# Kernel optimization log

Hardware: AMD Instinct MI355X
Metric: run time of the kernel (lower is better)

The kernel has to match this reference:

```python
import jax, jax.numpy as jnp
import numpy as np

N = 20000        # nodes
E = 320000       # edges (avg degree 16)
NHID = 256       # hidden dim (decoder input features)
NFEAT = 256      # reconstructed attribute dim
K_SELECTED = 4096  # number of nodes with label == 1 (static for jit)


def setup_inputs() -> dict:
    key = jax.random.key(0)
    ks = jax.random.split(key, 12)
    feature_attribute = jax.random.normal(ks[0], (N, NHID), dtype=jnp.float32)
    edge_row = jax.random.randint(ks[1], (E,), 0, N, dtype=jnp.int32)
    edge_col = jax.random.randint(ks[2], (E,), 0, N, dtype=jnp.int32)
    # positive, roughly degree-normalized adjacency weights
    edge_w = jax.random.uniform(ks[3], (E,), dtype=jnp.float32) / 16.0
    # first K_SELECTED nodes are labeled 1, rest 0 (static count for jit)
    labels = jnp.concatenate([jnp.ones((K_SELECTED,), jnp.int32),
                              jnp.zeros((N - K_SELECTED,), jnp.int32)])
    stdv1 = 1.0 / np.sqrt(NHID)
    stdv2 = 1.0 / np.sqrt(NFEAT)
    W1_ad = jax.random.uniform(ks[4], (NHID, NHID), minval=-stdv1, maxval=stdv1, dtype=jnp.float32)
    b1_ad = jax.random.uniform(ks[5], (NHID,), minval=-stdv1, maxval=stdv1, dtype=jnp.float32)
    W2_ad = jax.random.uniform(ks[6], (NHID, NFEAT), minval=-stdv2, maxval=stdv2, dtype=jnp.float32)
    b2_ad = jax.random.uniform(ks[7], (NFEAT,), minval=-stdv2, maxval=stdv2, dtype=jnp.float32)
    W_sd = jax.random.uniform(ks[8], (NHID, NHID), minval=-stdv1, maxval=stdv1, dtype=jnp.float32)
    b_sd = jax.random.uniform(ks[9], (NHID,), minval=-stdv1, maxval=stdv1, dtype=jnp.float32)
    return dict(feature_attribute=feature_attribute, edge_row=edge_row, edge_col=edge_col,
                edge_w=edge_w, labels=labels, W1_ad=W1_ad, b1_ad=b1_ad,
                W2_ad=W2_ad, b2_ad=b2_ad, W_sd=W_sd, b_sd=b_sd)


def reference(feature_attribute, edge_row, edge_col, edge_w, labels,
              W1_ad, b1_ad, W2_ad, b2_ad, W_sd, b_sd):
    def gcn(x, W, b):
        support = x @ W                                   # [N, d_out] dense mm
        msg = support[edge_col] * edge_w[:, None]         # gather + scale [E, d_out]
        out = jax.ops.segment_sum(msg, edge_row, num_segments=N)  # spmm aggregation
        return out + b

    # static-size index of labeled nodes (labels==1 count is K_SELECTED)
    idx = jnp.nonzero(labels == 1, size=K_SELECTED)[0]

    # Attribute decoder: relu(gc1) -> (dropout, eval: identity) -> gc2 -> select
    h = jax.nn.relu(gcn(feature_attribute, W1_ad, b1_ad))
    pred_attribute_mat = gcn(h, W2_ad, b2_ad)[idx]        # [K, NFEAT]

    # Structure decoder: gc1 -> select -> x @ x.T
    s = gcn(feature_attribute, W_sd, b_sd)[idx]           # [K, NHID]
    pred_adj_mat = s @ s.T                                # [K, K]

    return pred_attribute_mat, pred_adj_mat
```

## Files before the change

### kernel.cpp

```cpp
#include <hip/hip_runtime.h>
#include <hip/hip_bf16.h>

#define NN   20000
#define NE   320000
#define KSEL 4096

typedef short bf16x8 __attribute__((ext_vector_type(8)));
typedef float f32x4  __attribute__((ext_vector_type(4)));

static __device__ __forceinline__ float bf2f(unsigned short u){
  return __uint_as_float(((unsigned int)u) << 16);
}
static __device__ __forceinline__ unsigned short f2bf(float f){
  unsigned int x = __float_as_uint(f);
  x += 0x7fffu + ((x >> 16) & 1u);
  return (unsigned short)(x >> 16);
}
static __device__ __forceinline__ void gld_lds16(const unsigned short* g, unsigned short* l){
  __builtin_amdgcn_global_load_lds(
      (const __attribute__((address_space(1))) unsigned int*)g,
      (__attribute__((address_space(3))) unsigned int*)l, 16, 0, 0);
}

__global__ __launch_bounds__(256) void k_prep(const float* __restrict__ X,
    const float* __restrict__ W1, const float* __restrict__ Wsd, const float* __restrict__ W2,
    const int* __restrict__ labels,
    unsigned short* __restrict__ Xb, unsigned short* __restrict__ Wt,
    int* __restrict__ counts, int* __restrict__ partA){
  int b = blockIdx.x, tid = threadIdx.x;
  if (b < 2500){
    int i = (b * 256 + tid) * 8;
    float4 v0 = *(const float4*)(X + i);
    float4 v1 = *(const float4*)(X + i + 4);
    bf16x8 o;
    o[0] = (short)f2bf(v0.x); o[1] = (short)f2bf(v0.y);
    o[2] = (short)f2bf(v0.z); o[3] = (short)f2bf(v0.w);
    o[4] = (short)f2bf(v1.x); o[5] = (short)f2bf(v1.y);
    o[6] = (short)f2bf(v1.z); o[7] = (short)f2bf(v1.w);
    *(bf16x8*)(Xb + i) = o;
  } else if (b < 2548){
    __shared__ unsigned short lt[64 * 65];
    int b2 = b - 2500;
    int w = b2 >> 4, t = b2 & 15;
    int tR = (t >> 2) * 64, tC = (t & 3) * 64;
    const float* W = (w == 0) ? W1 : (w == 1 ? Wsd : W2);
    #pragma unroll
    for (int it = 0; it < 16; ++it){
      int lin = it * 256 + tid;
      int r = lin >> 6, c = lin & 63;
      lt[c * 65 + r] = f2bf(W[(size_t)(tR + r) * 256 + tC + c]);
    }
    __syncthreads();
    #pragma unroll
    for (int it = 0; it < 16; ++it){
      int lin = it * 256 + tid;
      int o = lin >> 6, k = lin & 63;
      Wt[(size_t)w * 65536 + (size_t)(tC + o) * 256 + tR + k] = lt[o * 65 + k];
    }
  } else {
    __shared__ int ws[4];
    int z = b - 2548, lane = tid & 63, wv = tid >> 6;
    if (tid < 250) *(int4*)&counts[z * 1000 + tid * 4] = make_int4(0, 0, 0, 0);
    int base = z * 1024 + tid * 4;
    int s = 0;
    #pragma unroll
    for (int j = 0; j < 4; ++j){
      int n0 = base + j;
      if (n0 < NN) s += (labels[n0] == 1) ? 1 : 0;
    }
    #pragma unroll
    for (int off = 32; off; off >>= 1) s += __shfl_down(s, off, 64);
    if (lane == 0) ws[wv] = s;
    __syncthreads();
    if (tid == 0) partA[z] = ws[0] + ws[1] + ws[2] + ws[3];
  }
}

__global__ __launch_bounds__(256) void k_hist_idx(const int* __restrict__ row,
    const int* __restrict__ labels, const int* __restrict__ partA,
    int* __restrict__ counts, int* __restrict__ idx){
  int tid = threadIdx.x;
  if (blockIdx.x < 1250){
    int e = blockIdx.x * 256 + tid;
    atomicAdd(&counts[row[e]], 1);
    return;
  }
  __shared__ int ws[4];
  __shared__ int boff_s;
  int bx = blockIdx.x - 1250;
  int lane = tid & 63, wv = tid >> 6;
  if (tid < 64){
    int v = (lane < 20) ? partA[lane] : 0;
    int acc = v;
    #pragma unroll
    for (int off = 1; off < 32; off <<= 1){
      int t = __shfl_up(acc, off, 64);
      if (lane >= off) acc += t;
    }
    if (lane == bx) boff_s = acc - v;
  }
  int base = bx * 1024 + tid * 4;
  int c[4]; int s = 0;
  #pragma unroll
  for (int j = 0; j < 4; ++j){
    int n0 = base + j;
    c[j] = (n0 < NN && labels[n0] == 1) ? 1 : 0;
    s += c[j];
  }
  int incl = s;
  #pragma unroll
  for (int off = 1; off < 64; off <<= 1){
    int t = __shfl_up(incl, off, 64);
    if (lane >= off) incl += t;
  }
  if (lane == 63) ws[wv] = incl;
  __syncthreads();
  int woff = boff_s;
  for (int w = 0; w < wv; ++w) woff += ws[w];
  int off = woff + incl - s;
  #pragma unroll
  for (int j = 0; j < 4; ++j){
    if (c[j]){ if (off < KSEL) idx[off] = base + j; ++off; }
  }
}

__global__ __launch_bounds__(256) void k_row_emit(const int* __restrict__ counts,
    int* __restrict__ start, int* __restrict__ cursor){
  __shared__ int ws[4];
  __shared__ int red[4];
  int tid = threadIdx.x, lane = tid & 63, wv = tid >> 6;
  int base = blockIdx.x * 1024;
  int ps = 0;
  for (int i = tid * 4; i < base; i += 1024){
    int4 v = *(const int4*)&counts[i];
    ps += v.x + v.y + v.z + v.w;
  }
  #pragma unroll
  for (int off = 32; off; off >>= 1) ps += __shfl_down(ps, off, 64);
  if (lane == 0) red[wv] = ps;
  __syncthreads();
  int bpref = red[0] + red[1] + red[2] + red[3];
  int nb = base + tid * 4;
  int c[4]; int s = 0;
  #pragma unroll
  for (int j = 0; j < 4; ++j){
    int n0 = nb + j;
    c[j] = (n0 < NN) ? counts[n0] : 0;
    s += c[j];
  }
  int incl = s;
  #pragma unroll
  for (int off = 1; off < 64; off <<= 1){
    int t = __shfl_up(incl, off, 64);
    if (lane >= off) incl += t;
  }
  if (lane == 63) ws[wv] = incl;
  __syncthreads();
  int woff = bpref;
  for (int w = 0; w < wv; ++w) woff += ws[w];
  int run = woff + incl - s;
  #pragma unroll
  for (int j = 0; j < 4; ++j){
    int n0 = nb + j;
    if (n0 < NN){ start[n0] = run; cursor[n0] = run; run += c[j]; }
  }
  if (blockIdx.x == 0 && tid == 0) start[NN] = NE;
}

__global__ void k_scatter(const int* __restrict__ row, const int* __restrict__ col,
                          const float* __restrict__ ew, int* __restrict__ cursor,
                          int2* __restrict__ rec){
  int e = blockIdx.x * 256 + threadIdx.x;
  if (e < NE){
    int r = row[e];
    int p = atomicAdd(&cursor[r], 1);
    rec[p] = make_int2(col[e], __float_as_int(ew[e]));
  }
}

__global__ __launch_bounds__(256) void k_spmm_full(const unsigned short* __restrict__ Xb,
    const int* __restrict__ start, const int2* __restrict__ rec,
    unsigned short* __restrict__ aggX){
  int wave = threadIdx.x >> 6, lane = threadIdx.x & 63;
  int half = lane >> 5, hl = lane & 31;
  int n = blockIdx.x * 4 + wave;
  int s = start[n], e = start[n + 1];
  int d = hl * 8;
  float acc[8] = {};
  for (int base = s; base < e; base += 64){
    int p = base + lane;
    int pc = p < e ? p : e - 1;
    int2 r = rec[pc];
    float wv = (p < e) ? __int_as_float(r.y) : 0.0f;
    int m = e - base; if (m > 64) m = 64;
    for (int j = 0; j < m; j += 8){
      int j0 = j + half, j1 = j + 2 + half, j2 = j + 4 + half, j3 = j + 6 + half;
      int   c0 = __shfl(r.x, j0), c1 = __shfl(r.x, j1);
      int   c2 = __shfl(r.x, j2), c3 = __shfl(r.x, j3);
      float w0 = __shfl(wv, j0),  w1 = __shfl(wv, j1);
      float w2 = __shfl(wv, j2),  w3 = __shfl(wv, j3);
      bf16x8 v0 = *(const bf16x8*)&Xb[(size_t)c0 * 256 + d];
      bf16x8 v1 = *(const bf16x8*)&Xb[(size_t)c1 * 256 + d];
      bf16x8 v2 = *(const bf16x8*)&Xb[(size_t)c2 * 256 + d];
      bf16x8 v3 = *(const bf16x8*)&Xb[(size_t)c3 * 256 + d];
      #pragma unroll
      for (int q = 0; q < 8; ++q){
        acc[q] += w0 * bf2f((unsigned short)v0[q]) + w1 * bf2f((unsigned short)v1[q])
                + w2 * bf2f((unsigned short)v2[q]) + w3 * bf2f((unsigned short)v3[q]);
      }
    }
  }
  #pragma unroll
  for (int q = 0; q < 8; ++q){
    float o = __shfl(acc[q], hl + 32);
    acc[q] += o;
  }
  if (half == 0){
    bf16x8 ob;
    #pragma unroll
    for (int q = 0; q < 8; ++q) ob[q] = (short)f2bf(acc[q]);
    *(bf16x8*)&aggX[(size_t)n * 256 + d] = ob;
  }
}

__global__ __launch_bounds__(256) void k_gemm_h(const unsigned short* __restrict__ A,
                                                const unsigned short* __restrict__ Wt,
                                                const float* __restrict__ bias,
                                                unsigned short* __restrict__ out, int M){
  __shared__ unsigned short At[128 * 64];
  __shared__ unsigned short Bt[64 * 64];
  int tid = threadIdx.x, wave = tid >> 6, lane = tid & 63;
  int lm = lane & 15, lq = lane >> 4;
  int mBase = blockIdx.x * 128;
  int oBase = blockIdx.y * 64;
  f32x4 acc[2][4] = {};
  for (int kc = 0; kc < 256; kc += 64){
    if (kc) __syncthreads();
    #pragma unroll
    for (int it = 0; it < 4; ++it){
      int s = (wave * 4 + it) * 64 + lane;
      int row = s >> 3, c = (s & 7) ^ (row & 7);
      int gr = mBase + row; if (gr >= M) gr = M - 1;
      gld_lds16(&A[(size_t)gr * 256 + kc + c * 8], &At[s * 8]);
    }
    #pragma unroll
    for (int it = 0; it < 2; ++it){
      int s = (wave * 2 + it) * 64 + lane;
      int row = s >> 3, c = (s & 7) ^ (row & 7);
      gld_lds16(&Wt[(size_t)(oBase + row) * 256 + kc + c * 8], &Bt[s * 8]);
    }
    __syncthreads();
    #pragma unroll
    for (int ks = 0; ks < 64; ks += 32){
      int cb = ks >> 3;
      int RA = wave * 32 + lm;
      int ca = ((cb + lq) ^ (RA & 7)) << 3;
      bf16x8 a0 = *(const bf16x8*)&At[RA * 64 + ca];
      bf16x8 a1 = *(const bf16x8*)&At[(RA + 16) * 64 + ca];
      #pragma unroll
      for (int os = 0; os < 4; ++os){
        int RB = os * 16 + lm;
        bf16x8 b = *(const bf16x8*)&Bt[RB * 64 + (((cb + lq) ^ (RB & 7)) << 3)];
        acc[0][os] = __builtin_amdgcn_mfma_f32_16x16x32_bf16(a0, b, acc[0][os], 0, 0, 0);
        acc[1][os] = __builtin_amdgcn_mfma_f32_16x16x32_bf16(a1, b, acc[1][os], 0, 0, 0);
      }
    }
  }
  #pragma unroll
  for (int ms = 0; ms < 2; ++ms){
    int rb = mBase + wave * 32 + ms * 16 + lq * 4;
    #pragma unroll
    for (int os = 0; os < 4; ++os){
      int col = oBase + os * 16 + lm;
      float bv = bias[col];
      #pragma unroll
      for (int r = 0; r < 4; ++r){
        int row = rb + r;
        if (row < M) out[(size_t)row * 256 + col] = f2bf(fmaxf(acc[ms][os][r] + bv, 0.f));
      }
    }
  }
}

__global__ __launch_bounds__(256) void k_spmm_selH(const unsigned short* __restrict__ h,
    const int* __restrict__ idx, const int* __restrict__ start, const int2* __restrict__ rec,
    unsigned short* __restrict__ aggH){
  int wave = threadIdx.x >> 6, lane = threadIdx.x & 63;
  int half = lane >> 5, hl = lane & 31;
  int i = blockIdx.x * 4 + wave;
  int n = idx[i];
  int s = start[n], e = start[n + 1];
  int d = hl * 8;
  float acc[8] = {};
  for (int base = s; base < e; base += 64){
    int p = base + lane;
    int pc = p < e ? p : e - 1;
    int2 r = rec[pc];
    float wv = (p < e) ? __int_as_float(r.y) : 0.0f;
    int m = e - base; if (m > 64) m = 64;
    for (int j = 0; j < m; j += 8){
      int j0 = j + half, j1 = j + 2 + half, j2 = j + 4 + half, j3 = j + 6 + half;
      int   c0 = __shfl(r.x, j0), c1 = __shfl(r.x, j1);
      int   c2 = __shfl(r.x, j2), c3 = __shfl(r.x, j3);
      float w0 = __shfl(wv, j0),  w1 = __shfl(wv, j1);
      float w2 = __shfl(wv, j2),  w3 = __shfl(wv, j3);
      bf16x8 v0 = *(const bf16x8*)&h[(size_t)c0 * 256 + d];
      bf16x8 v1 = *(const bf16x8*)&h[(size_t)c1 * 256 + d];
      bf16x8 v2 = *(const bf16x8*)&h[(size_t)c2 * 256 + d];
      bf16x8 v3 = *(const bf16x8*)&h[(size_t)c3 * 256 + d];
      #pragma unroll
      for (int q = 0; q < 8; ++q){
        acc[q] += w0 * bf2f((unsigned short)v0[q]) + w1 * bf2f((unsigned short)v1[q])
                + w2 * bf2f((unsigned short)v2[q]) + w3 * bf2f((unsigned short)v3[q]);
      }
    }
  }
  #pragma unroll
  for (int q = 0; q < 8; ++q){
    float o = __shfl(acc[q], hl + 32);
    acc[q] += o;
  }
  if (half == 0){
    bf16x8 ob;
    #pragma unroll
    for (int q = 0; q < 8; ++q) ob[q] = (short)f2bf(acc[q]);
    *(bf16x8*)&aggH[(size_t)i * 256 + d] = ob;
  }
}

__global__ __launch_bounds__(256) void k_gemm_os(const unsigned short* __restrict__ aggH,
    const unsigned short* __restrict__ aggX, const int* __restrict__ idx,
    const unsigned short* __restrict__ Wt,
    const float* __restrict__ b2, const float* __restrict__ bsd,
    float* __restrict__ out0, unsigned short* __restrict__ sel){
  __shared__ unsigned short lds[64 * 264];
  int tid = threadIdx.x;
  int wave = tid >> 6, lane = tid & 63;
  int lm = lane & 15, lq = lane >> 4;
  int z = blockIdx.z;
  int mBase = blockIdx.x * 128;
  int oBase = blockIdx.y * 64;
  const unsigned short* Wt2 = Wt + (z ? 256 * 256 : 512 * 256);
  const float* bias = z ? bsd : b2;
  #pragma unroll
  for (int it = 0; it < 8; ++it){
    int c = it * 256 + tid;
    int o = c >> 5, kk = (c & 31) << 3;
    *(bf16x8*)&lds[o * 264 + kk] = *(const bf16x8*)&Wt2[(oBase + o) * 256 + kk];
  }
  __syncthreads();
  int r0 = mBase + wave * 32 + lm;
  const unsigned short* A0;
  const unsigned short* A1;
  if (z){
    A0 = aggX + (size_t)idx[r0] * 256;
    A1 = aggX + (size_t)idx[r0 + 16] * 256;
  } else {
    A0 = aggH + (size_t)r0 * 256;
    A1 = aggH + (size_t)(r0 + 16) * 256;
  }
  f32x4 acc[2][4] = {};
  #pragma unroll
  for (int ks = 0; ks < 256; ks += 32){
    int ka = ks + lq * 8;
    bf16x8 a0 = *(const bf16x8*)&A0[ka];
    bf16x8 a1 = *(const bf16x8*)&A1[ka];
    #pragma unroll
    for (int os = 0; os < 4; ++os){
      bf16x8 b = *(const bf16x8*)&lds[(os * 16 + lm) * 264 + ka];
      acc[0][os] = __builtin_amdgcn_mfma_f32_16x16x32_bf16(a0, b, acc[0][os], 0, 0, 0);
      acc[1][os] = __builtin_amdgcn_mfma_f32_16x16x32_bf16(a1, b, acc[1][os], 0, 0, 0);
    }
  }
  #pragma unroll
  for (int ms = 0; ms < 2; ++ms){
    int rb = mBase + wave * 32 + ms * 16 + lq * 4;
    #pragma unroll
    for (int os = 0; os < 4; ++os){
      int col = oBase + os * 16 + lm;
      float bv = bias[col];
      #pragma unroll
      for (int r = 0; r < 4; ++r){
        float v = acc[ms][os][r] + bv;
        if (z) sel[(size_t)(rb + r) * 256 + col] = f2bf(v);
        else   out0[(size_t)(rb + r) * 256 + col] = v;
      }
    }
  }
}

__global__ __launch_bounds__(256) void k_gemm_st(const unsigned short* __restrict__ S,
                                                 float* __restrict__ out1){
  __shared__ unsigned short At[128 * 64];
  __shared__ unsigned short Bt[128 * 64];
  int tid = threadIdx.x, wave = tid >> 6, lane = tid & 63;
  int lm = lane & 15, lq = lane >> 4;
  int mBase = blockIdx.x * 128;
  int oBase = blockIdx.y * 128;
  f32x4 acc[2][8] = {};
  for (int kc = 0; kc < 256; kc += 64){
    if (kc) __syncthreads();
    #pragma unroll
    for (int it = 0; it < 4; ++it){
      int s = (wave * 4 + it) * 64 + lane;
      int row = s >> 3, c = (s & 7) ^ (row & 7);
      gld_lds16(&S[(size_t)(mBase + row) * 256 + kc + c * 8], &At[s * 8]);
      gld_lds16(&S[(size_t)(oBase + row) * 256 + kc + c * 8], &Bt[s * 8]);
    }
    __syncthreads();
    #pragma unroll
    for (int ks = 0; ks < 64; ks += 32){
      int cb = ks >> 3;
      int RA = wave * 32 + lm;
      int ca = ((cb + lq) ^ (RA & 7)) << 3;
      bf16x8 a0 = *(const bf16x8*)&At[RA * 64 + ca];
      bf16x8 a1 = *(const bf16x8*)&At[(RA + 16) * 64 + ca];
      #pragma unroll
      for (int os = 0; os < 8; ++os){
        int RB = os * 16 + lm;
        bf16x8 b = *(const bf16x8*)&Bt[RB * 64 + (((cb + lq) ^ (RB & 7)) << 3)];
        acc[0][os] = __builtin_amdgcn_mfma_f32_16x16x32_bf16(a0, b, acc[0][os], 0, 0, 0);
        acc[1][os] = __builtin_amdgcn_mfma_f32_16x16x32_bf16(a1, b, acc[1][os], 0, 0, 0);
      }
    }
  }
  #pragma unroll
  for (int ms = 0; ms < 2; ++ms){
    int rb = mBase + wave * 32 + ms * 16 + lq * 4;
    #pragma unroll
    for (int os = 0; os < 8; ++os){
      int col = oBase + os * 16 + lm;
      #pragma unroll
      for (int r = 0; r < 4; ++r)
        out1[(size_t)(rb + r) * 4096 + col] = acc[ms][os][r];
    }
  }
}

extern "C" void kernel_launch(void* const* d_in, const int* in_sizes, int n_in,
                              void* d_out, int out_size, void* d_ws, size_t ws_size,
                              hipStream_t stream){
  const float* X    = (const float*)d_in[0];
  const int*   erow = (const int*)d_in[1];
  const int*   ecol = (const int*)d_in[2];
  const float* ew   = (const float*)d_in[3];
  const int*   labels = (const int*)d_in[4];
  const float* W1   = (const float*)d_in[5];
  const float* b1   = (const float*)d_in[6];
  const float* W2   = (const float*)d_in[7];
  const float* b2   = (const float*)d_in[8];
  const float* Wsd  = (const float*)d_in[9];
  const float* bsd  = (const float*)d_in[10];
  float* out0 = (float*)d_out;
  float* out1 = out0 + (size_t)KSEL * 256;

  char* ws = (char*)d_ws;
  unsigned short* Xb   = (unsigned short*)(ws);
  unsigned short* Wt   = (unsigned short*)(ws + 10240000);
  unsigned short* aggX = (unsigned short*)(ws + 10633216);
  unsigned short* h    = (unsigned short*)(ws + 20873216);
  unsigned short* aggH = (unsigned short*)(ws + 31113216);
  unsigned short* sel  = (unsigned short*)(ws + 33210368);
  int* idx    = (int*)(ws + 35307520);
  int* counts = (int*)(ws + 35323904);
  int* startp = (int*)(ws + 35403904);
  int* cursor = (int*)(ws + 35483908);
  int2* rec   = (int2*)(ws + 35563912);
  int* partA  = (int*)(ws + 38123912);

  k_prep<<<2568, 256, 0, stream>>>(X, W1, Wsd, W2, labels, Xb, Wt, counts, partA);
  k_hist_idx<<<1270, 256, 0, stream>>>(erow, labels, partA, counts, idx);
  k_row_emit<<<20, 256, 0, stream>>>(counts, startp, cursor);
  k_scatter<<<NE / 256, 256, 0, stream>>>(erow, ecol, ew, cursor, rec);
  k_spmm_full<<<5000, 256, 0, stream>>>(Xb, startp, rec, aggX);
  k_gemm_h<<<dim3(157, 4), 256, 0, stream>>>(aggX, Wt, b1, h, NN);
  k_spmm_selH<<<1024, 256, 0, stream>>>(h, idx, startp, rec, aggH);
  k_gemm_os<<<dim3(32, 4, 2), 256, 0, stream>>>(aggH, aggX, idx, Wt, b2, bsd, out0, sel);
  k_gemm_st<<<dim3(32, 32), 256, 0, stream>>>(sel, out1);
}
```

Measured before the change: 203.8 us.

## Merge kernels into fewer launches and exploit Gram-matrix symmetry

The setup kernels are regrouped so that the X-to-bf16 conversion, the edge histogram and the index compaction run in one launch, with the weight transpose split into a small separate kernel. The selected-row Wsd GEMM is fused into the selected SpMM launch, and the W2 output GEMM into the S·Sᵀ launch. The K×K Gram matrix now computes only lower-triangular 128×128 tiles and writes each off-diagonal tile a second time in transposed form through LDS. These changes remove launch gaps and about half of the Gram-matrix MFMA work. The fused output GEMMs now read B directly from global memory instead of staging it in LDS, which may cost some bandwidth.

```diff
diff --git a/kernel.cpp b/kernel.cpp
--- a/kernel.cpp
+++ b/kernel.cpp
@@ -22,11 +22,52 @@
       (__attribute__((address_space(3))) unsigned int*)l, 16, 0, 0);
 }
 
-__global__ __launch_bounds__(256) void k_prep(const float* __restrict__ X,
-    const float* __restrict__ W1, const float* __restrict__ Wsd, const float* __restrict__ W2,
+__global__ __launch_bounds__(256) void k_prep0(const float* __restrict__ W1,
+    const float* __restrict__ Wsd, const float* __restrict__ W2,
     const int* __restrict__ labels,
-    unsigned short* __restrict__ Xb, unsigned short* __restrict__ Wt,
-    int* __restrict__ counts, int* __restrict__ partA){
+    unsigned short* __restrict__ Wt, int* __restrict__ counts, int* __restrict__ partA){
+  int b = blockIdx.x, tid = threadIdx.x;
+  if (b < 48){
+    __shared__ unsigned short lt[64 * 65];
+    int w = b >> 4, t = b & 15;
+    int tR = (t >> 2) * 64, tC = (t & 3) * 64;
+    const float* W = (w == 0) ? W1 : (w == 1 ? Wsd : W2);
+    #pragma unroll
+    for (int it = 0; it < 16; ++it){
+      int lin = it * 256 + tid;
+      int r = lin >> 6, c = lin & 63;
+      lt[c * 65 + r] = f2bf(W[(size_t)(tR + r) * 256 + tC + c]);
+    }
+    __syncthreads();
+    #pragma unroll
+    for (int it = 0; it < 16; ++it){
+      int lin = it * 256 + tid;
+      int o = lin >> 6, k = lin & 63;
+      Wt[(size_t)w * 65536 + (size_t)(tC + o) * 256 + tR + k] = lt[o * 65 + k];
+    }
+  } else {
+    __shared__ int ws[4];
+    int z = b - 48, lane = tid & 63, wv = tid >> 6;
+    if (tid < 250) *(int4*)&counts[z * 1000 + tid * 4] = make_int4(0, 0, 0, 0);
+    int base = z * 1024 + tid * 4;
+    int s = 0;
+    #pragma unroll
+    for (int j = 0; j < 4; ++j){
+      int n0 = base + j;
+      if (n0 < NN) s += (labels[n0] == 1) ? 1 : 0;
+    }
+    #pragma unroll
+    for (int off = 32; off; off >>= 1) s += __shfl_down(s, off, 64);
+    if (lane == 0) ws[wv] = s;
+    __syncthreads();
+    if (tid == 0) partA[z] = ws[0] + ws[1] + ws[2] + ws[3];
+  }
+}
+
+__global__ __launch_bounds__(256) void k_main1(const float* __restrict__ X,
+    const int* __restrict__ row, const int* __restrict__ labels,
+    const int* __restrict__ partA,
+    unsigned short* __restrict__ Xb, int* __restrict__ counts, int* __restrict__ idx){
   int b = blockIdx.x, tid = threadIdx.x;
   if (b < 2500){
     int i = (b * 256 + tid) * 8;
@@ -38,89 +79,47 @@
     o[4] = (short)f2bf(v1.x); o[5] = (short)f2bf(v1.y);
     o[6] = (short)f2bf(v1.z); o[7] = (short)f2bf(v1.w);
     *(bf16x8*)(Xb + i) = o;
-  } else if (b < 2548){
-    __shared__ unsigned short lt[64 * 65];
-    int b2 = b - 2500;
-    int w = b2 >> 4, t = b2 & 15;
-    int tR = (t >> 2) * 64, tC = (t & 3) * 64;
-    const float* W = (w == 0) ? W1 : (w == 1 ? Wsd : W2);
-    #pragma unroll
-    for (int it = 0; it < 16; ++it){
-      int lin = it * 256 + tid;
-      int r = lin >> 6, c = lin & 63;
-      lt[c * 65 + r] = f2bf(W[(size_t)(tR + r) * 256 + tC + c]);
-    }
-    __syncthreads();
-    #pragma unroll
-    for (int it = 0; it < 16; ++it){
-      int lin = it * 256 + tid;
-      int o = lin >> 6, k = lin & 63;
-      Wt[(size_t)w * 65536 + (size_t)(tC + o) * 256 + tR + k] = lt[o * 65 + k];
-    }
+  } else if (b < 3750){
+    int e = (b - 2500) * 256 + tid;
+    atomicAdd(&counts[row[e]], 1);
   } else {
     __shared__ int ws[4];
-    int z = b - 2548, lane = tid & 63, wv = tid >> 6;
-    if (tid < 250) *(int4*)&counts[z * 1000 + tid * 4] = make_int4(0, 0, 0, 0);
-    int base = z * 1024 + tid * 4;
-    int s = 0;
+    __shared__ int boff_s;
+    int bx = b - 3750;
+    int lane = tid & 63, wv = tid >> 6;
+    if (tid < 64){
+      int v = (lane < 20) ? partA[lane] : 0;
+      int acc = v;
+      #pragma unroll
+      for (int off = 1; off < 32; off <<= 1){
+        int t = __shfl_up(acc, off, 64);
+        if (lane >= off) acc += t;
+      }
+      if (lane == bx) boff_s = acc - v;
+    }
+    int base = bx * 1024 + tid * 4;
+    int c[4]; int s = 0;
     #pragma unroll
     for (int j = 0; j < 4; ++j){
       int n0 = base + j;
-      if (n0 < NN) s += (labels[n0] == 1) ? 1 : 0;
-    }
-    #pragma unroll
-    for (int off = 32; off; off >>= 1) s += __shfl_down(s, off, 64);
-    if (lane == 0) ws[wv] = s;
-    __syncthreads();
-    if (tid == 0) partA[z] = ws[0] + ws[1] + ws[2] + ws[3];
-  }
-}
-
-__global__ __launch_bounds__(256) void k_hist_idx(const int* __restrict__ row,
-    const int* __restrict__ labels, const int* __restrict__ partA,
-    int* __restrict__ counts, int* __restrict__ idx){
-  int tid = threadIdx.x;
-  if (blockIdx.x < 1250){
-    int e = blockIdx.x * 256 + tid;
-    atomicAdd(&counts[row[e]], 1);
-    return;
-  }
-  __shared__ int ws[4];
-  __shared__ int boff_s;
-  int bx = blockIdx.x - 1250;
-  int lane = tid & 63, wv = tid >> 6;
-  if (tid < 64){
-    int v = (lane < 20) ? partA[lane] : 0;
-    int acc = v;
-    #pragma unroll
-    for (int off = 1; off < 32; off <<= 1){
-      int t = __shfl_up(acc, off, 64);
-      if (lane >= off) acc += t;
-    }
-    if (lane == bx) boff_s = acc - v;
-  }
-  int base = bx * 1024 + tid * 4;
-  int c[4]; int s = 0;
-  #pragma unroll
-  for (int j = 0; j < 4; ++j){
-    int n0 = base + j;
-    c[j] = (n0 < NN && labels[n0] == 1) ? 1 : 0;
-    s += c[j];
-  }
-  int incl = s;
-  #pragma unroll
-  for (int off = 1; off < 64; off <<= 1){
-    int t = __shfl_up(incl, off, 64);
-    if (lane >= off) incl += t;
-  }
-  if (lane == 63) ws[wv] = incl;
-  __syncthreads();
-  int woff = boff_s;
-  for (int w = 0; w < wv; ++w) woff += ws[w];
-  int off = woff + incl - s;
-  #pragma unroll
-  for (int j = 0; j < 4; ++j){
-    if (c[j]){ if (off < KSEL) idx[off] = base + j; ++off; }
+      c[j] = (n0 < NN && labels[n0] == 1) ? 1 : 0;
+      s += c[j];
+    }
+    int incl = s;
+    #pragma unroll
+    for (int off = 1; off < 64; off <<= 1){
+      int t = __shfl_up(incl, off, 64);
+      if (lane >= off) incl += t;
+    }
+    if (lane == 63) ws[wv] = incl;
+    __syncthreads();
+    int woff = boff_s;
+    for (int w = 0; w < wv; ++w) woff += ws[w];
+    int off = woff + incl - s;
+    #pragma unroll
+    for (int j = 0; j < 4; ++j){
+      if (c[j]){ if (off < KSEL) idx[off] = base + j; ++off; }
+    }
   }
 }
 
@@ -282,12 +281,49 @@
   }
 }
 
-__global__ __launch_bounds__(256) void k_spmm_selH(const unsigned short* __restrict__ h,
+__global__ __launch_bounds__(256) void k_tail1(const unsigned short* __restrict__ h,
     const int* __restrict__ idx, const int* __restrict__ start, const int2* __restrict__ rec,
-    unsigned short* __restrict__ aggH){
-  int wave = threadIdx.x >> 6, lane = threadIdx.x & 63;
+    unsigned short* __restrict__ aggH, const unsigned short* __restrict__ aggX,
+    const unsigned short* __restrict__ Wt, const float* __restrict__ bsd,
+    unsigned short* __restrict__ sel){
+  int tid = threadIdx.x, wave = tid >> 6, lane = tid & 63;
+  if (blockIdx.x < 128){
+    int lm = lane & 15, lq = lane >> 4;
+    int b2 = blockIdx.x;
+    int mBase = (b2 & 31) * 128, oBase = (b2 >> 5) * 64;
+    const unsigned short* W = Wt + 256 * 256;
+    int r0 = mBase + wave * 32 + lm;
+    const unsigned short* A0 = aggX + (size_t)idx[r0] * 256;
+    const unsigned short* A1 = aggX + (size_t)idx[r0 + 16] * 256;
+    f32x4 acc[2][4] = {};
+    #pragma unroll
+    for (int ks = 0; ks < 256; ks += 32){
+      int ka = ks + lq * 8;
+      bf16x8 a0 = *(const bf16x8*)&A0[ka];
+      bf16x8 a1 = *(const bf16x8*)&A1[ka];
+      #pragma unroll
+      for (int os = 0; os < 4; ++os){
+        bf16x8 b = *(const bf16x8*)&W[(size_t)(oBase + os * 16 + lm) * 256 + ka];
+        acc[0][os] = __builtin_amdgcn_mfma_f32_16x16x32_bf16(a0, b, acc[0][os], 0, 0, 0);
+        acc[1][os] = __builtin_amdgcn_mfma_f32_16x16x32_bf16(a1, b, acc[1][os], 0, 0, 0);
+      }
+    }
+    #pragma unroll
+    for (int ms = 0; ms < 2; ++ms){
+      int rb = mBase + wave * 32 + ms * 16 + lq * 4;
+      #pragma unroll
+      for (int os = 0; os < 4; ++os){
+        int col = oBase + os * 16 + lm;
+        float bv = bsd[col];
+        #pragma unroll
+        for (int r = 0; r < 4; ++r)
+          sel[(size_t)(rb + r) * 256 + col] = f2bf(acc[ms][os][r] + bv);
+      }
+    }
+    return;
+  }
   int half = lane >> 5, hl = lane & 31;
-  int i = blockIdx.x * 4 + wave;
+  int i = (blockIdx.x - 128) * 4 + wave;
   int n = idx[i];
   int s = start[n], e = start[n + 1];
   int d = hl * 8;
@@ -328,75 +364,54 @@
   }
 }
 
-__global__ __launch_bounds__(256) void k_gemm_os(const unsigned short* __restrict__ aggH,
-    const unsigned short* __restrict__ aggX, const int* __restrict__ idx,
-    const unsigned short* __restrict__ Wt,
-    const float* __restrict__ b2, const float* __restrict__ bsd,
-    float* __restrict__ out0, unsigned short* __restrict__ sel){
-  __shared__ unsigned short lds[64 * 264];
-  int tid = threadIdx.x;
-  int wave = tid >> 6, lane = tid & 63;
-  int lm = lane & 15, lq = lane >> 4;
-  int z = blockIdx.z;
-  int mBase = blockIdx.x * 128;
-  int oBase = blockIdx.y * 64;
-  const unsigned short* Wt2 = Wt + (z ? 256 * 256 : 512 * 256);
-  const float* bias = z ? bsd : b2;
-  #pragma unroll
-  for (int it = 0; it < 8; ++it){
-    int c = it * 256 + tid;
-    int o = c >> 5, kk = (c & 31) << 3;
-    *(bf16x8*)&lds[o * 264 + kk] = *(const bf16x8*)&Wt2[(oBase + o) * 256 + kk];
-  }
-  __syncthreads();
-  int r0 = mBase + wave * 32 + lm;
-  const unsigned short* A0;
-  const unsigned short* A1;
-  if (z){
-    A0 = aggX + (size_t)idx[r0] * 256;
-    A1 = aggX + (size_t)idx[r0 + 16] * 256;
-  } else {
-    A0 = aggH + (size_t)r0 * 256;
-    A1 = aggH + (size_t)(r0 + 16) * 256;
-  }
-  f32x4 acc[2][4] = {};
-  #pragma unroll
-  for (int ks = 0; ks < 256; ks += 32){
-    int ka = ks + lq * 8;
-    bf16x8 a0 = *(const bf16x8*)&A0[ka];
-    bf16x8 a1 = *(const bf16x8*)&A1[ka];
-    #pragma unroll
-    for (int os = 0; os < 4; ++os){
-      bf16x8 b = *(const bf16x8*)&lds[(os * 16 + lm) * 264 + ka];
-      acc[0][os] = __builtin_amdgcn_mfma_f32_16x16x32_bf16(a0, b, acc[0][os], 0, 0, 0);
-      acc[1][os] = __builtin_amdgcn_mfma_f32_16x16x32_bf16(a1, b, acc[1][os], 0, 0, 0);
-    }
-  }
-  #pragma unroll
-  for (int ms = 0; ms < 2; ++ms){
-    int rb = mBase + wave * 32 + ms * 16 + lq * 4;
-    #pragma unroll
-    for (int os = 0; os < 4; ++os){
-      int col = oBase + os * 16 + lm;
-      float bv = bias[col];
-      #pragma unroll
-      for (int r = 0; r < 4; ++r){
-        float v = acc[ms][os][r] + bv;
-        if (z) sel[(size_t)(rb + r) * 256 + col] = f2bf(v);
-        else   out0[(size_t)(rb + r) * 256 + col] = v;
-      }
-    }
-  }
-}
-
-__global__ __launch_bounds__(256) void k_gemm_st(const unsigned short* __restrict__ S,
-                                                 float* __restrict__ out1){
-  __shared__ unsigned short At[128 * 64];
-  __shared__ unsigned short Bt[128 * 64];
+__global__ __launch_bounds__(256) void k_tail2(const unsigned short* __restrict__ aggH,
+    const unsigned short* __restrict__ Wt, const float* __restrict__ b2v,
+    float* __restrict__ out0, const unsigned short* __restrict__ S,
+    float* __restrict__ out1){
+  __shared__ __align__(16) char smem[34816];
   int tid = threadIdx.x, wave = tid >> 6, lane = tid & 63;
   int lm = lane & 15, lq = lane >> 4;
-  int mBase = blockIdx.x * 128;
-  int oBase = blockIdx.y * 128;
+  if (blockIdx.x < 128){
+    int b2 = blockIdx.x;
+    int mBase = (b2 & 31) * 128, oBase = (b2 >> 5) * 64;
+    const unsigned short* W = Wt + 512 * 256;
+    const unsigned short* A0 = aggH + (size_t)(mBase + wave * 32 + lm) * 256;
+    const unsigned short* A1 = A0 + 16 * 256;
+    f32x4 acc[2][4] = {};
+    #pragma unroll
+    for (int ks = 0; ks < 256; ks += 32){
+      int ka = ks + lq * 8;
+      bf16x8 a0 = *(const bf16x8*)&A0[ka];
+      bf16x8 a1 = *(const bf16x8*)&A1[ka];
+      #pragma unroll
+      for (int os = 0; os < 4; ++os){
+        bf16x8 b = *(const bf16x8*)&W[(size_t)(oBase + os * 16 + lm) * 256 + ka];
+        acc[0][os] = __builtin_amdgcn_mfma_f32_16x16x32_bf16(a0, b, acc[0][os], 0, 0, 0);
+        acc[1][os] = __builtin_amdgcn_mfma_f32_16x16x32_bf16(a1, b, acc[1][os], 0, 0, 0);
+      }
+    }
+    #pragma unroll
+    for (int ms = 0; ms < 2; ++ms){
+      int rb = mBase + wave * 32 + ms * 16 + lq * 4;
+      #pragma unroll
+      for (int os = 0; os < 4; ++os){
+        int col = oBase + os * 16 + lm;
+        float bv = b2v[col];
+        #pragma unroll
+        for (int r = 0; r < 4; ++r)
+          out0[(size_t)(rb + r) * 256 + col] = acc[ms][os][r] + bv;
+      }
+    }
+    return;
+  }
+  int t = blockIdx.x - 128;
+  int bx = (int)((sqrtf(8.f * (float)t + 1.f) - 1.f) * 0.5f);
+  while ((bx + 1) * (bx + 2) / 2 <= t) ++bx;
+  while (bx * (bx + 1) / 2 > t) --bx;
+  int by = t - bx * (bx + 1) / 2;
+  int mBase = bx * 128, oBase = by * 128;
+  unsigned short* At = (unsigned short*)smem;
+  unsigned short* Bt = (unsigned short*)(smem + 16384);
   f32x4 acc[2][8] = {};
   for (int kc = 0; kc < 256; kc += 64){
     if (kc) __syncthreads();
@@ -433,6 +448,29 @@
       #pragma unroll
       for (int r = 0; r < 4; ++r)
         out1[(size_t)(rb + r) * 4096 + col] = acc[ms][os][r];
+    }
+  }
+  if (bx == by) return;
+  float* fst = (float*)smem;
+  #pragma unroll
+  for (int half = 0; half < 2; ++half){
+    __syncthreads();
+    #pragma unroll
+    for (int ms = 0; ms < 2; ++ms){
+      int mr = wave * 32 + ms * 16 + lq * 4;
+      #pragma unroll
+      for (int os2 = 0; os2 < 4; ++os2){
+        int oc = os2 * 16 + lm;
+        *(f32x4*)&fst[oc * 136 + mr] = acc[ms][half * 4 + os2];
+      }
+    }
+    __syncthreads();
+    int l = tid & 31, ocb = tid >> 5;
+    #pragma unroll
+    for (int it = 0; it < 8; ++it){
+      int oc = it * 8 + ocb;
+      f32x4 v = *(const f32x4*)&fst[oc * 136 + l * 4];
+      *(f32x4*)&out1[(size_t)(oBase + half * 64 + oc) * 4096 + mBase + l * 4] = v;
     }
   }
 }
@@ -468,13 +506,12 @@
   int2* rec   = (int2*)(ws + 35563912);
   int* partA  = (int*)(ws + 38123912);
 
-  k_prep<<<2568, 256, 0, stream>>>(X, W1, Wsd, W2, labels, Xb, Wt, counts, partA);
-  k_hist_idx<<<1270, 256, 0, stream>>>(erow, labels, partA, counts, idx);
+  k_prep0<<<68, 256, 0, stream>>>(W1, Wsd, W2, labels, Wt, counts, partA);
+  k_main1<<<3770, 256, 0, stream>>>(X, erow, labels, partA, Xb, counts, idx);
   k_row_emit<<<20, 256, 0, stream>>>(counts, startp, cursor);
-  k_scatter<<<NE / 256, 256, 0, stream>>>(erow, ecol, ew, cursor, rec);
+  k_scatter<<<1250, 256, 0, stream>>>(erow, ecol, ew, cursor, rec);
   k_spmm_full<<<5000, 256, 0, stream>>>(Xb, startp, rec, aggX);
   k_gemm_h<<<dim3(157, 4), 256, 0, stream>>>(aggX, Wt, b1, h, NN);
-  k_spmm_selH<<<1024, 256, 0, stream>>>(h, idx, startp, rec, aggH);
-  k_gemm_os<<<dim3(32, 4, 2), 256, 0, stream>>>(aggH, aggX, idx, Wt, b2, bsd, out0, sel);
-  k_gemm_st<<<dim3(32, 32), 256, 0, stream>>>(sel, out1);
-}
+  k_tail1<<<1152, 256, 0, stream>>>(h, idx, startp, rec, aggH, aggX, Wt, bsd, sel);
+  k_tail2<<<656, 256, 0, stream>>>(aggH, Wt, b2, out0, sel, out1);
+}
```

Result: no change. 203.5 us (-0.1%).
